# Kernel tuning notes

Hardware: AMD Instinct MI355X
Metric: run time of the kernel (lower is better)

The kernel has to match this reference:

```python
import jax, jax.numpy as jnp
import numpy as np

N_NODES = 100000
N_EDGES = 1600000
EPS = 1e-12  # F.normalize eps


def _lin(key, i, o):
    return jax.random.normal(key, (i, o), jnp.float32) * 0.05


def setup_inputs() -> dict:
    key = jax.random.key(0)
    ks = jax.random.split(key, 16)
    inp = {
        'x': jax.random.normal(ks[0], (N_NODES, 100), jnp.float32),
        'edge_index': jax.random.randint(ks[1], (2, N_EDGES), 0, N_NODES, dtype=jnp.int64),
        'edge_weight': jax.random.uniform(ks[2], (N_EDGES,), jnp.float32),
        'emb_W': _lin(ks[3], 100, 80), 'emb_b': jnp.zeros((80,), jnp.float32),
        'Wl0': _lin(ks[4], 80, 64), 'Wr0': _lin(ks[5], 80, 64), 'b0': jnp.zeros((64,), jnp.float32),
        'Wl1': _lin(ks[6], 64, 64), 'Wr1': _lin(ks[7], 64, 64), 'b1': jnp.zeros((64,), jnp.float32),
        'Wl2': _lin(ks[8], 64, 64), 'Wr2': _lin(ks[9], 64, 64), 'b2': jnp.zeros((64,), jnp.float32),
        'Wl3': _lin(ks[10], 64, 64), 'Wr3': _lin(ks[11], 64, 64), 'b3': jnp.zeros((64,), jnp.float32),
        'Wlo': _lin(ks[12], 64, 18), 'Wro': _lin(ks[13], 64, 18), 'bo': jnp.zeros((18,), jnp.float32),
    }
    return inp


def _sage_conv(x, src, dst, ew, Wl, Wr, b):
    # message: edge_weight * x_j, mean-aggregated onto dst nodes
    msg = x[src] * ew[:, None]                                   # [E, C]
    agg = jax.ops.segment_sum(msg, dst, num_segments=N_NODES)    # [N, C]
    deg = jax.ops.segment_sum(jnp.ones_like(ew), dst, num_segments=N_NODES)
    agg = agg / jnp.maximum(deg, 1.0)[:, None]
    out = agg @ Wl + x @ Wr + b
    nrm = jnp.linalg.norm(out, axis=-1, keepdims=True)
    return out / jnp.maximum(nrm, EPS)                           # L2 normalize


def reference(x, edge_index, edge_weight, emb_W, emb_b,
              Wl0, Wr0, b0, Wl1, Wr1, b1, Wl2, Wr2, b2, Wl3, Wr3, b3,
              Wlo, Wro, bo):
    src, dst = edge_index[0], edge_index[1]
    h = jax.nn.relu(x @ emb_W + emb_b)                           # embedding
    ones_w = jnp.ones_like(edge_weight)
    for Wl, Wr, b in ((Wl0, Wr0, b0), (Wl1, Wr1, b1), (Wl2, Wr2, b2), (Wl3, Wr3, b3)):
        h = _sage_conv(h, src, dst, edge_weight, Wl, Wr, b)
        h = jax.nn.relu(h)
        # dropout(p=0.2) is identity in eval mode
    h = _sage_conv(h, src, dst, ones_w, Wlo, Wro, bo)            # out layer (no edge_weight)
    return h
```

## Files before the change

kernel.cpp:

```cpp
#include <hip/hip_runtime.h>
#include <hip/hip_bf16.h>

#define N_NODES 100000
#define N_EDGES 1600000
#define SCAN_BLOCKS ((N_NODES+255)/256)

using bf16 = __hip_bfloat16;
typedef unsigned int u32;
typedef __attribute__((ext_vector_type(8))) short short8;
typedef __attribute__((ext_vector_type(4))) float f32x4;

static __device__ __forceinline__ float b2f(bf16 v){ return __bfloat162float(v); }

static __device__ __forceinline__ float ldf(const void* p, long i, int f32m){
  return f32m ? ((const float*)p)[i] : b2f(((const bf16*)p)[i]);
}

static __device__ __forceinline__ u32 f2bf_rne(float f){
  u32 b = __float_as_uint(f);
  return (b + 0x7fffu + ((b>>16)&1u)) >> 16;
}

__global__ void k_detect(const u32* __restrict__ xw, const int* __restrict__ eiw,
                         int* __restrict__ flags){
  __shared__ int s_wild, s_nzodd;
  if(threadIdx.x==0){ s_wild=0; s_nzodd=0; }
  __syncthreads();
  int wild=0, nz=0;
  for(int k=threadIdx.x;k<2048;k+=256){
    u32 w  = xw[k];
    u32 lo = w & 0xffffu;
    int e  = (int)((lo>>7)&0xffu);
    if((lo & 0x7fffu)!=0u && (e<90 || e>160)) wild++;
    if(eiw[2*k+1]!=0) nz++;
  }
  atomicAdd(&s_wild, wild);
  atomicAdd(&s_nzodd, nz);
  __syncthreads();
  if(threadIdx.x==0){
    flags[0] = (s_wild > 512) ? 1 : 0;
    flags[1] = (s_nzodd == 0) ? 1 : 0;
  }
}

__global__ void k_zero2(int* __restrict__ a, int* __restrict__ b){
  int i = blockIdx.x*256 + threadIdx.x;
  if(i<N_NODES){ a[i]=0; b[i]=0; }
}


__global__ void k_count(const int* __restrict__ ei, const int* __restrict__ flags,
                        int* __restrict__ deg){
  int e = blockIdx.x*256 + threadIdx.x;
  int i64 = flags[1];
  if(e < N_EDGES){
    long di = i64 ? 2l*(N_EDGES + e) : (long)(N_EDGES + e);
    atomicAdd(&deg[ei[di]], 1);
  }
}

__global__ void k_scan1(const int* __restrict__ deg, int* __restrict__ off,
                        int* __restrict__ bsum){
  const int t = threadIdx.x, lane = t&63, wid = t>>6;
  const int i = blockIdx.x*256 + t;
  int v = (i<N_NODES) ? deg[i] : 0;
  const int orig = v;
  #pragma unroll
  for(int d=1; d<64; d<<=1){ int u = __shfl_up(v,d); if(lane>=d) v += u; }
  __shared__ int wsum[4];
  if(lane==63) wsum[wid] = v;
  __syncthreads();
  int wbase = 0;
  for(int k=0;k<wid;k++) wbase += wsum[k];
  if(i<N_NODES) off[i] = wbase + v - orig;
  if(t==255) bsum[blockIdx.x] = wbase + v;
}

__global__ void k_scan2(const int* __restrict__ bsum, int* __restrict__ bbase){
  const int t = threadIdx.x, lane = t&63, wid = t>>6;
  int v = (t<SCAN_BLOCKS) ? bsum[t] : 0;
  const int orig = v;
  #pragma unroll
  for(int d=1; d<64; d<<=1){ int u = __shfl_up(v,d); if(lane>=d) v += u; }
  __shared__ int wsum[8];
  if(lane==63) wsum[wid] = v;
  __syncthreads();
  int wbase = 0;
  for(int k=0;k<wid;k++) wbase += wsum[k];
  if(t<SCAN_BLOCKS) bbase[t] = wbase + v - orig;
}

__global__ void k_scan3(int* __restrict__ off, const int* __restrict__ bbase){
  const int i = blockIdx.x*256 + threadIdx.x;
  if(i<N_NODES) off[i] += bbase[blockIdx.x];
  if(i==0) off[N_NODES] = N_EDGES;
}

__global__ void k_fill(const int* __restrict__ ei, const void* __restrict__ ew,
                       const int* __restrict__ flags, const int* __restrict__ off,
                       int* __restrict__ cur, uint2* __restrict__ csr){
  int e = blockIdx.x*256 + threadIdx.x;
  int i64 = flags[1], f32m = flags[0];
  if(e < N_EDGES){
    int s = ei[i64 ? 2l*e : (long)e];
    int d = ei[i64 ? 2l*(N_EDGES+e) : (long)(N_EDGES+e)];
    int p = atomicAdd(&cur[d], 1);
    int idx = off[d] + p;
    csr[idx] = make_uint2((u32)s, __float_as_uint(ldf(ew, e, f32m)));
  }
}


__global__ void k_packb(const void* __restrict__ Wl, const void* __restrict__ Wr,
                        const int* __restrict__ flags, int CIN, int COUT,
                        int KT, int NT, short* __restrict__ out){
  int idx = blockIdx.x*256 + threadIdx.x;
  int total = KT*NT*512;
  if(idx < total){
    int jj = idx & 7;
    int l  = (idx>>3) & 63;
    int tile = idx >> 9;
    int nt = tile % NT, kt = tile / NT;
    int k   = kt*32 + ((l>>4)<<3) + jj;
    int col = nt*16 + (l&15);
    int khalf = (KT/2)*32;
    float v = 0.f;
    if(col < COUT){
      int f32m = flags[0];
      if(k < khalf){ if(k < CIN) v = ldf(Wl,(long)k*COUT+col,f32m); }
      else { int ch = k - khalf; if(ch < CIN) v = ldf(Wr,(long)ch*COUT+col,f32m); }
    }
    out[idx] = (short)f2bf_rne(v);
  }
}


__global__ __launch_bounds__(256,2) void k_embed(const void* __restrict__ x,
                                                 const void* __restrict__ W,
                                                 const void* __restrict__ b,
                                                 const int* __restrict__ flags,
                                                 float* __restrict__ h){
  __shared__ float xs[100][65];
  __shared__ float Ws[100*80];
  const int t = threadIdx.x;
  const int n0 = blockIdx.x*64;
  const int f32m = flags[0];
  for(int i=t;i<8000;i+=256) Ws[i]=ldf(W,i,f32m);
  for(int idx=t; idx<6400; idx+=256){
    int n = idx/100, c = idx - n*100;
    float v = (n0+n < N_NODES) ? ldf(x,(long)(n0+n)*100+c,f32m) : 0.f;
    xs[c][n] = v;
  }
  __syncthreads();

  const int ng = t&15, og = t>>4;
  float acc[4][5];
  #pragma unroll
  for(int j=0;j<5;j++){
    float bj = ldf(b, og*5+j, f32m);
    #pragma unroll
    for(int i=0;i<4;i++) acc[i][j] = bj;
  }
  #pragma unroll 2
  for(int c=0;c<100;c++){
    float xv[4];
    #pragma unroll
    for(int i=0;i<4;i++) xv[i] = xs[c][ng*4+i];
    #pragma unroll
    for(int j=0;j<5;j++){
      float wj = Ws[c*80+og*5+j];
      #pragma unroll
      for(int i=0;i<4;i++) acc[i][j] = fmaf(xv[i], wj, acc[i][j]);
    }
  }
  #pragma unroll
  for(int i=0;i<4;i++){
    int n = n0 + ng*4 + i;
    if(n < N_NODES){
      #pragma unroll
      for(int j=0;j<5;j++) h[(long)n*80 + og*5+j] = fmaxf(acc[i][j], 0.f);
    }
  }
}


template<int CIN, int COUT, bool LAST>
__global__ __launch_bounds__(256,4) void k_sage(
    const float* __restrict__ hin, const int* __restrict__ off,
    const uint2* __restrict__ csr,
    const short* __restrict__ Wb, const void* __restrict__ bias,
    const int* __restrict__ flags, float* __restrict__ hout, void* __restrict__ outp)
{
  constexpr int KHT  = (CIN+31)/32;
  constexpr int KT   = 2*KHT;
  constexpr int NT   = (COUT+15)/16;
  constexpr int ROWB = KT*32*2;
  constexpr int LPE  = CIN/4;
  constexpr int EPW  = 64/LPE;

  __shared__ char smem[4*16*ROWB];

  const int f32m = flags[0];
  const int lane = threadIdx.x&63, wid = threadIdx.x>>6;
  const int wnode0 = blockIdx.x*64 + wid*16;
  char* lds = smem + wid*16*ROWB;

  const int sub = lane/LPE;
  const int cl  = lane - sub*LPE;
  const bool lact = (sub < EPW);

  for(int tt=0; tt<16; ++tt){
    const int node = wnode0 + tt;
    if(node >= N_NODES) continue;

    float ax=0.f, ay=0.f, az=0.f, aw=0.f;
    const int e0 = off[node], e1 = off[node+1];
    for(int base=e0; base<e1; base+=64){
      const int cnt = min(64, e1-base);
      uint2 ev = (lane<cnt) ? csr[base+lane] : make_uint2(0u,0u);
      int   sv = (int)ev.x;
      float wv = LAST ? 1.f : __uint_as_float(ev.y);
      for(int j=0; j<cnt; j+=4*EPW){
        int ei0 = j+sub, ei1 = j+EPW+sub, ei2 = j+2*EPW+sub, ei3 = j+3*EPW+sub;
        bool v0 = lact && (ei0<cnt), v1 = lact && (ei1<cnt);
        bool v2 = lact && (ei2<cnt), v3 = lact && (ei3<cnt);
        int x0 = v0?ei0:0, x1 = v1?ei1:0, x2 = v2?ei2:0, x3 = v3?ei3:0;
        int   s0=__shfl(sv,x0), s1=__shfl(sv,x1), s2=__shfl(sv,x2), s3=__shfl(sv,x3);
        float w0=__shfl(wv,x0)*(v0?1.f:0.f), w1=__shfl(wv,x1)*(v1?1.f:0.f);
        float w2=__shfl(wv,x2)*(v2?1.f:0.f), w3=__shfl(wv,x3)*(v3?1.f:0.f);
        const float4 r0 = *(const float4*)(hin + (long)s0*CIN + 4*cl);
        const float4 r1 = *(const float4*)(hin + (long)s1*CIN + 4*cl);
        const float4 r2 = *(const float4*)(hin + (long)s2*CIN + 4*cl);
        const float4 r3 = *(const float4*)(hin + (long)s3*CIN + 4*cl);
        ax = fmaf(w0,r0.x, fmaf(w1,r1.x, fmaf(w2,r2.x, fmaf(w3,r3.x, ax))));
        ay = fmaf(w0,r0.y, fmaf(w1,r1.y, fmaf(w2,r2.y, fmaf(w3,r3.y, ay))));
        az = fmaf(w0,r0.z, fmaf(w1,r1.z, fmaf(w2,r2.z, fmaf(w3,r3.z, az))));
        aw = fmaf(w0,r0.w, fmaf(w1,r1.w, fmaf(w2,r2.w, fmaf(w3,r3.w, aw))));
      }
    }

    if(EPW == 4){
      ax += __shfl_xor(ax,16); ax += __shfl_xor(ax,32);
      ay += __shfl_xor(ay,16); ay += __shfl_xor(ay,32);
      az += __shfl_xor(az,16); az += __shfl_xor(az,32);
      aw += __shfl_xor(aw,16); aw += __shfl_xor(aw,32);
    } else {
      ax = __shfl(ax,cl) + __shfl(ax,cl+20) + __shfl(ax,cl+40);
      ay = __shfl(ay,cl) + __shfl(ay,cl+20) + __shfl(ay,cl+40);
      az = __shfl(az,cl) + __shfl(az,cl+20) + __shfl(az,cl+40);
      aw = __shfl(aw,cl) + __shfl(aw,cl+20) + __shfl(aw,cl+40);
    }
    const float inv = 1.f/fmaxf((float)(e1-e0), 1.f);

    const int sx = (tt&7)<<4;
    if(lane < LPE){
      u32 lo = f2bf_rne(ax*inv) | (f2bf_rne(ay*inv)<<16);
      u32 hi = f2bf_rne(az*inv) | (f2bf_rne(aw*inv)<<16);
      int ob = tt*ROWB + lane*8;
      *(uint2*)(lds + (ob^sx)) = make_uint2(lo,hi);
    }
    const float* hs = hin + (long)__builtin_amdgcn_readfirstlane(node)*CIN;
    if(lane < CIN/2){
      float2 hv = *(const float2*)(hs + 2*lane);
      u32 pk = f2bf_rne(hv.x) | (f2bf_rne(hv.y)<<16);
      int ob = tt*ROWB + KHT*64 + lane*4;
      *(u32*)(lds + (ob^sx)) = pk;
    }
    if(CIN==80){
      if(lane>=20 && lane<24){
        int ob = tt*ROWB + 160 + (lane-20)*8;
        *(uint2*)(lds + (ob^sx)) = make_uint2(0u,0u);
      }
      if(lane>=40 && lane<48){
        int ob = tt*ROWB + 352 + (lane-40)*4;
        *(u32*)(lds + (ob^sx)) = 0u;
      }
    }
  }

  f32x4 acc[NT];
  #pragma unroll
  for(int nt=0; nt<NT; ++nt){
    int col = nt*16 + (lane&15);
    float bv = (col<COUT) ? ldf(bias,col,f32m) : 0.f;
    acc[nt] = (f32x4){bv,bv,bv,bv};
  }
  const int arow = lane&15, kgrp = lane>>4;
  #pragma unroll
  for(int kt=0; kt<KT; ++kt){
    int ob = arow*ROWB + kt*64 + kgrp*16;
    short8 a8 = *(const short8*)(lds + (ob ^ ((arow&7)<<4)));
    #pragma unroll
    for(int nt=0; nt<NT; ++nt){
      short8 b8 = *(const short8*)(Wb + ((long)(kt*NT+nt)*64 + lane)*8);
      acc[nt] = __builtin_amdgcn_mfma_f32_16x16x32_bf16(a8, b8, acc[nt], 0,0,0);
    }
  }

  float sq[4];
  #pragma unroll
  for(int r=0;r<4;r++){
    float s = 0.f;
    #pragma unroll
    for(int nt=0;nt<NT;nt++){ float v = acc[nt][r]; s = fmaf(v,v,s); }
    #pragma unroll
    for(int d=1; d<16; d<<=1) s += __shfl_xor(s, d);
    sq[r] = s;
  }
  #pragma unroll
  for(int r=0;r<4;r++){
    float rn = 1.f/fmaxf(sqrtf(sq[r]), 1e-12f);
    const int node = wnode0 + 4*(lane>>4) + r;
    #pragma unroll
    for(int nt=0;nt<NT;nt++){
      int col = nt*16 + (lane&15);
      float v = acc[nt][r]*rn;
      if(!LAST) v = fmaxf(v,0.f);
      if(node < N_NODES && col < COUT){
        if(LAST){
          long oi = (long)node*COUT + col;
          if(f32m) ((float*)outp)[oi] = v;
          else     ((bf16*)outp)[oi]  = __float2bfloat16(v);
        } else {
          hout[(long)node*64 + col] = v;
        }
      }
    }
  }
}


extern "C" void kernel_launch(void* const* d_in, const int* in_sizes, int n_in,
                              void* d_out, int out_size, void* d_ws, size_t ws_size,
                              hipStream_t stream){
  const void* x    = d_in[0];
  const int*  ei   = (const int*)d_in[1];
  const void* ew   = d_in[2];
  const void* embW = d_in[3];
  const void* embB = d_in[4];
  const void *Wl0=d_in[5],  *Wr0=d_in[6],  *b0=d_in[7];
  const void *Wl1=d_in[8],  *Wr1=d_in[9],  *b1=d_in[10];
  const void *Wl2=d_in[11], *Wr2=d_in[12], *b2=d_in[13];
  const void *Wl3=d_in[14], *Wr3=d_in[15], *b3=d_in[16];
  const void *Wlo=d_in[17], *Wro=d_in[18], *bo=d_in[19];

  char* w = (char*)d_ws;
  auto carve = [&](size_t nbytes)->char*{
    char* r = w; w += (nbytes + 255) & ~(size_t)255; return r;
  };
  int*   flags   = (int*)carve(16);
  int*   deg     = (int*)carve((size_t)N_NODES*4);
  int*   cur     = (int*)carve((size_t)N_NODES*4);
  int*   off     = (int*)carve((size_t)(N_NODES+1)*4);
  int*   bsum    = (int*)carve((size_t)SCAN_BLOCKS*4);
  int*   bbase   = (int*)carve((size_t)SCAN_BLOCKS*4);
  uint2* csr     = (uint2*)carve((size_t)N_EDGES*8);
  short* Wb0     = (short*)carve((size_t)6*4*512*2);
  short* Wb1     = (short*)carve((size_t)4*4*512*2);
  short* Wb2     = (short*)carve((size_t)4*4*512*2);
  short* Wb3     = (short*)carve((size_t)4*4*512*2);
  short* Wbo     = (short*)carve((size_t)4*2*512*2);
  float* hA      = (float*)carve((size_t)N_NODES*80*4);
  float* hB      = (float*)carve((size_t)N_NODES*64*4);

  k_detect<<<1, 256, 0, stream>>>((const u32*)x, ei, flags);
  k_zero2<<<(N_NODES+255)/256, 256, 0, stream>>>(deg, cur);
  k_count<<<N_EDGES/256, 256, 0, stream>>>(ei, flags, deg);
  k_scan1<<<SCAN_BLOCKS, 256, 0, stream>>>(deg, off, bsum);
  k_scan2<<<1, 512, 0, stream>>>(bsum, bbase);
  k_scan3<<<SCAN_BLOCKS, 256, 0, stream>>>(off, bbase);
  k_fill <<<N_EDGES/256, 256, 0, stream>>>(ei, ew, flags, off, cur, csr);

  k_packb<<<48, 256, 0, stream>>>(Wl0, Wr0, flags, 80, 64, 6, 4, Wb0);
  k_packb<<<32, 256, 0, stream>>>(Wl1, Wr1, flags, 64, 64, 4, 4, Wb1);
  k_packb<<<32, 256, 0, stream>>>(Wl2, Wr2, flags, 64, 64, 4, 4, Wb2);
  k_packb<<<32, 256, 0, stream>>>(Wl3, Wr3, flags, 64, 64, 4, 4, Wb3);
  k_packb<<<16, 256, 0, stream>>>(Wlo, Wro, flags, 64, 18, 4, 2, Wbo);

  k_embed<<<(N_NODES+63)/64, 256, 0, stream>>>(x, embW, embB, flags, hA);

  const int NBLK = (N_NODES+63)/64;
  k_sage<80,64,false><<<NBLK, 256, 0, stream>>>(hA, off, csr, Wb0, b0, flags, hB, nullptr);
  k_sage<64,64,false><<<NBLK, 256, 0, stream>>>(hB, off, csr, Wb1, b1, flags, hA, nullptr);
  k_sage<64,64,false><<<NBLK, 256, 0, stream>>>(hA, off, csr, Wb2, b2, flags, hB, nullptr);
  k_sage<64,64,false><<<NBLK, 256, 0, stream>>>(hB, off, csr, Wb3, b3, flags, hA, nullptr);
  k_sage<64,18,true ><<<NBLK, 256, 0, stream>>>(hA, off, csr, Wbo, bo, flags, nullptr, d_out);
}
```

Before: 651.2 us.

## Partition CSR fill by XCD, vectorize embed loads, shrink sage blocks

The CSR fill launches 8x as many blocks, and each block handles only edges whose destination falls in its XCD's node range, so atomics and scattered writes stay within one L2 slice. The cost is that each edge's dst index is read eight times. The embedding kernel now reads weights straight from a pre-converted fp32 global buffer instead of staging them in LDS, and loads x with vectorized float4 or packed bf16 loads. The sage kernels move to 128-thread blocks covering 32 nodes each, which raises the block count and lowers LDS per block to allow more resident blocks.

```diff
diff --git a/kernel.cpp b/kernel.cpp
--- a/kernel.cpp
+++ b/kernel.cpp
@@ -48,6 +48,15 @@
   if(i<N_NODES){ a[i]=0; b[i]=0; }
 }
 
+__global__ void k_cvt(const void* __restrict__ W, const void* __restrict__ b,
+                      const int* __restrict__ flags, float* __restrict__ Wo,
+                      float* __restrict__ bo_){
+  int i = blockIdx.x*256 + threadIdx.x;
+  int f32m = flags[0];
+  if(i<8000) Wo[i] = ldf(W,i,f32m);
+  if(i<80)   bo_[i] = ldf(b,i,f32m);
+}
+
 
 __global__ void k_count(const int* __restrict__ ei, const int* __restrict__ flags,
                         int* __restrict__ deg){
@@ -99,14 +108,16 @@
 __global__ void k_fill(const int* __restrict__ ei, const void* __restrict__ ew,
                        const int* __restrict__ flags, const int* __restrict__ off,
                        int* __restrict__ cur, uint2* __restrict__ csr){
-  int e = blockIdx.x*256 + threadIdx.x;
-  int i64 = flags[1], f32m = flags[0];
+  const int xcd = blockIdx.x & 7;
+  const int e = (blockIdx.x>>3)*256 + threadIdx.x;
+  const int i64 = flags[1], f32m = flags[0];
   if(e < N_EDGES){
-    int s = ei[i64 ? 2l*e : (long)e];
     int d = ei[i64 ? 2l*(N_EDGES+e) : (long)(N_EDGES+e)];
-    int p = atomicAdd(&cur[d], 1);
-    int idx = off[d] + p;
-    csr[idx] = make_uint2((u32)s, __float_as_uint(ldf(ew, e, f32m)));
+    if(d/12500 == xcd){
+      int s = ei[i64 ? 2l*e : (long)e];
+      int p = atomicAdd(&cur[d], 1);
+      csr[off[d]+p] = make_uint2((u32)s, __float_as_uint(ldf(ew, e, f32m)));
+    }
   }
 }
 
@@ -135,21 +146,30 @@
 }
 
 
-__global__ __launch_bounds__(256,2) void k_embed(const void* __restrict__ x,
-                                                 const void* __restrict__ W,
-                                                 const void* __restrict__ b,
-                                                 const int* __restrict__ flags,
-                                                 float* __restrict__ h){
+__global__ __launch_bounds__(256) void k_embed(const void* __restrict__ x,
+                                               const float* __restrict__ W,
+                                               const float* __restrict__ b,
+                                               const int* __restrict__ flags,
+                                               float* __restrict__ h){
   __shared__ float xs[100][65];
-  __shared__ float Ws[100*80];
   const int t = threadIdx.x;
   const int n0 = blockIdx.x*64;
-  const int f32m = flags[0];
-  for(int i=t;i<8000;i+=256) Ws[i]=ldf(W,i,f32m);
-  for(int idx=t; idx<6400; idx+=256){
-    int n = idx/100, c = idx - n*100;
-    float v = (n0+n < N_NODES) ? ldf(x,(long)(n0+n)*100+c,f32m) : 0.f;
-    xs[c][n] = v;
+  if(flags[0]){
+    const float* xf = (const float*)x;
+    for(int idx=t; idx<1600; idx+=256){
+      int n = idx/25, q = idx-25*(idx/25);
+      float4 v = (n0+n < N_NODES) ? *(const float4*)(xf + (long)(n0+n)*100 + 4*q)
+                                  : make_float4(0.f,0.f,0.f,0.f);
+      xs[4*q+0][n]=v.x; xs[4*q+1][n]=v.y; xs[4*q+2][n]=v.z; xs[4*q+3][n]=v.w;
+    }
+  } else {
+    const u32* xu = (const u32*)x;
+    for(int idx=t; idx<3200; idx+=256){
+      int n = idx/50, q = idx-50*(idx/50);
+      u32 v = (n0+n < N_NODES) ? xu[(long)(n0+n)*50 + q] : 0u;
+      xs[2*q+0][n]=__uint_as_float(v<<16);
+      xs[2*q+1][n]=__uint_as_float(v&0xffff0000u);
+    }
   }
   __syncthreads();
 
@@ -157,7 +177,7 @@
   float acc[4][5];
   #pragma unroll
   for(int j=0;j<5;j++){
-    float bj = ldf(b, og*5+j, f32m);
+    float bj = b[og*5+j];
     #pragma unroll
     for(int i=0;i<4;i++) acc[i][j] = bj;
   }
@@ -168,7 +188,7 @@
     for(int i=0;i<4;i++) xv[i] = xs[c][ng*4+i];
     #pragma unroll
     for(int j=0;j<5;j++){
-      float wj = Ws[c*80+og*5+j];
+      float wj = W[c*80+og*5+j];
       #pragma unroll
       for(int i=0;i<4;i++) acc[i][j] = fmaf(xv[i], wj, acc[i][j]);
     }
@@ -185,7 +205,7 @@
 
 
 template<int CIN, int COUT, bool LAST>
-__global__ __launch_bounds__(256,4) void k_sage(
+__global__ __launch_bounds__(128,6) void k_sage(
     const float* __restrict__ hin, const int* __restrict__ off,
     const uint2* __restrict__ csr,
     const short* __restrict__ Wb, const void* __restrict__ bias,
@@ -198,11 +218,11 @@
   constexpr int LPE  = CIN/4;
   constexpr int EPW  = 64/LPE;
 
-  __shared__ char smem[4*16*ROWB];
+  __shared__ char smem[2*16*ROWB];
 
   const int f32m = flags[0];
   const int lane = threadIdx.x&63, wid = threadIdx.x>>6;
-  const int wnode0 = blockIdx.x*64 + wid*16;
+  const int wnode0 = blockIdx.x*32 + wid*16;
   char* lds = smem + wid*16*ROWB;
 
   const int sub = lane/LPE;
@@ -360,6 +380,8 @@
   short* Wb2     = (short*)carve((size_t)4*4*512*2);
   short* Wb3     = (short*)carve((size_t)4*4*512*2);
   short* Wbo     = (short*)carve((size_t)4*2*512*2);
+  float* Wef     = (float*)carve((size_t)8000*4);
+  float* bef     = (float*)carve((size_t)80*4);
   float* hA      = (float*)carve((size_t)N_NODES*80*4);
   float* hB      = (float*)carve((size_t)N_NODES*64*4);
 
@@ -369,20 +391,21 @@
   k_scan1<<<SCAN_BLOCKS, 256, 0, stream>>>(deg, off, bsum);
   k_scan2<<<1, 512, 0, stream>>>(bsum, bbase);
   k_scan3<<<SCAN_BLOCKS, 256, 0, stream>>>(off, bbase);
-  k_fill <<<N_EDGES/256, 256, 0, stream>>>(ei, ew, flags, off, cur, csr);
-
+  k_fill <<<8*(N_EDGES/256), 256, 0, stream>>>(ei, ew, flags, off, cur, csr);
+
+  k_cvt  <<<32, 256, 0, stream>>>(embW, embB, flags, Wef, bef);
   k_packb<<<48, 256, 0, stream>>>(Wl0, Wr0, flags, 80, 64, 6, 4, Wb0);
   k_packb<<<32, 256, 0, stream>>>(Wl1, Wr1, flags, 64, 64, 4, 4, Wb1);
   k_packb<<<32, 256, 0, stream>>>(Wl2, Wr2, flags, 64, 64, 4, 4, Wb2);
   k_packb<<<32, 256, 0, stream>>>(Wl3, Wr3, flags, 64, 64, 4, 4, Wb3);
   k_packb<<<16, 256, 0, stream>>>(Wlo, Wro, flags, 64, 18, 4, 2, Wbo);
 
-  k_embed<<<(N_NODES+63)/64, 256, 0, stream>>>(x, embW, embB, flags, hA);
-
-  const int NBLK = (N_NODES+63)/64;
-  k_sage<80,64,false><<<NBLK, 256, 0, stream>>>(hA, off, csr, Wb0, b0, flags, hB, nullptr);
-  k_sage<64,64,false><<<NBLK, 256, 0, stream>>>(hB, off, csr, Wb1, b1, flags, hA, nullptr);
-  k_sage<64,64,false><<<NBLK, 256, 0, stream>>>(hA, off, csr, Wb2, b2, flags, hB, nullptr);
-  k_sage<64,64,false><<<NBLK, 256, 0, stream>>>(hB, off, csr, Wb3, b3, flags, hA, nullptr);
-  k_sage<64,18,true ><<<NBLK, 256, 0, stream>>>(hA, off, csr, Wbo, bo, flags, nullptr, d_out);
-}
+  k_embed<<<(N_NODES+63)/64, 256, 0, stream>>>(x, Wef, bef, flags, hA);
+
+  const int NBLK = (N_NODES+31)/32;
+  k_sage<80,64,false><<<NBLK, 128, 0, stream>>>(hA, off, csr, Wb0, b0, flags, hB, nullptr);
+  k_sage<64,64,false><<<NBLK, 128, 0, stream>>>(hB, off, csr, Wb1, b1, flags, hA, nullptr);
+  k_sage<64,64,false><<<NBLK, 128, 0, stream>>>(hA, off, csr, Wb2, b2, flags, hB, nullptr);
+  k_sage<64,64,false><<<NBLK, 128, 0, stream>>>(hB, off, csr, Wb3, b3, flags, hA, nullptr);
+  k_sage<64,18,true ><<<NBLK, 128, 0, stream>>>(hA, off, csr, Wbo, bo, flags, nullptr, d_out);
+}
```

Measured after the change: 570.9 us. 12.3% less time.
